# Kernel optimization log

Measured on AMD Instinct MI355X. Metric: run time of the kernel, lower is better.

Reference implementation:

```python
import jax, jax.numpy as jnp
import numpy as np

HID = 256; NH = 8; DH = 32; NL = 2
NV = 20000; NT = 50000; NE = 100000; NC = 8; FIN = 64


def setup_inputs() -> dict:
    ks = jax.random.split(jax.random.key(0), 32)
    f = lambda i, sh, s: jax.random.normal(ks[i], sh, dtype=jnp.float32) * s
    return {
        "x_v": f(0, (NV, FIN), 1.0),
        "x_t": f(1, (NT, FIN), 1.0),
        "ei_vt_src": jax.random.randint(ks[2], (NE,), 0, NV),
        "ei_vt_dst": jax.random.randint(ks[3], (NE,), 0, NT),
        "ei_tv_src": jax.random.randint(ks[4], (NE,), 0, NT),
        "ei_tv_dst": jax.random.randint(ks[5], (NE,), 0, NV),
        "ei_tt_src": jax.random.randint(ks[6], (NE,), 0, NT),
        "ei_tt_dst": jax.random.randint(ks[7], (NE,), 0, NT),
        "current": jax.random.randint(ks[8], (NC, 2), 0, NV),
        "W_in_v": f(9, (FIN, HID), 0.05), "b_in_v": jnp.zeros((HID,)),
        "W_in_t": f(10, (FIN, HID), 0.05), "b_in_t": jnp.zeros((HID,)),
        "Wk": f(11, (NL, 2, HID, HID), 0.05), "bk": jnp.zeros((NL, 2, HID)),
        "Wq": f(12, (NL, 2, HID, HID), 0.05), "bq": jnp.zeros((NL, 2, HID)),
        "Wv": f(13, (NL, 2, HID, HID), 0.05), "bv": jnp.zeros((NL, 2, HID)),
        "Wa": f(14, (NL, 2, HID, HID), 0.05), "ba": jnp.zeros((NL, 2, HID)),
        "skip": jnp.zeros((NL, 2)),
        "a_rel": f(15, (NL, 3, NH, DH, DH), 0.1),
        "m_rel": f(16, (NL, 3, NH, DH, DH), 0.1),
        "p_rel": jnp.ones((NL, 3, NH)),
        "Ws1": f(17, (2 * HID, HID), 0.05), "bs1": jnp.zeros((HID,)),
        "Ws2": f(18, (HID, 2), 0.05), "bs2": jnp.zeros((2,)),
    }


def reference(x_v, x_t, ei_vt_src, ei_vt_dst, ei_tv_src, ei_tv_dst,
              ei_tt_src, ei_tt_dst, current,
              W_in_v, b_in_v, W_in_t, b_in_t,
              Wk, bk, Wq, bq, Wv, bv, Wa, ba, skip,
              a_rel, m_rel, p_rel, Ws1, bs1, Ws2, bs2):
    scale = 1.0 / jnp.sqrt(jnp.float32(DH))
    # input projections + relu (lin_dict)
    hv = jax.nn.relu(x_v @ W_in_v + b_in_v)
    ht = jax.nn.relu(x_t @ W_in_t + b_in_t)
    # edge types: (src_type, dst_type, rel_idx, src_idx, dst_idx); 0=vehicle, 1=track
    edges = [(0, 1, 0, ei_vt_src, ei_vt_dst),
             (1, 0, 1, ei_tv_src, ei_tv_dst),
             (1, 1, 2, ei_tt_src, ei_tt_dst)]
    for l in range(NL):
        h = (hv, ht)
        proj = lambda W, b, t: (h[t] @ W[l, t] + b[l, t]).reshape(-1, NH, DH)
        k = (proj(Wk, bk, 0), proj(Wk, bk, 1))
        q = (proj(Wq, bq, 0), proj(Wq, bq, 1))
        v = (proj(Wv, bv, 0), proj(Wv, bv, 1))
        agg = [jnp.zeros((NV, NH, DH), jnp.float32),
               jnp.zeros((NT, NH, DH), jnp.float32)]
        for (st, dt, r, si, di) in edges:
            nd = agg[dt].shape[0]
            ke = jnp.einsum('ehd,hdf->ehf', k[st][si], a_rel[l, r])  # [E,H,D]
            ve = jnp.einsum('ehd,hdf->ehf', v[st][si], m_rel[l, r])  # [E,H,D]
            logit = (q[dt][di] * ke).sum(-1) * p_rel[l, r] * scale    # [E,H]
            m = jax.ops.segment_max(logit, di, num_segments=nd)
            e = jnp.exp(logit - m[di])
            s = jax.ops.segment_sum(e, di, num_segments=nd)
            alpha = e / (s[di] + 1e-16)
            agg[dt] = agg[dt] + jax.ops.segment_sum(alpha[..., None] * ve, di,
                                                    num_segments=nd)
        new = []
        for t in (0, 1):
            o = jax.nn.gelu(agg[t].reshape(-1, HID), approximate=False) @ Wa[l, t] + ba[l, t]
            beta = jax.nn.sigmoid(skip[l, t])
            new.append(beta * o + (1.0 - beta) * h[t])
        hv, ht = new
    # batched Scorer over (current vehicles) x (all tracks); cat([track, vehicle])
    veh = hv[current[:, 0]]                 # [C,HID]
    tpart = ht @ Ws1[:HID]                  # [NT,HID]
    vpart = veh @ Ws1[HID:] + bs1           # [C,HID]
    hmid = jax.nn.relu(tpart[None, :, :] + vpart[:, None, :])  # [C,NT,HID]
    out = hmid @ Ws2 + bs2                  # [C,NT,2]
    return out[..., 0], jax.nn.sigmoid(out[..., 1])
```

## Files before the change

### kernel.cpp

```cpp
#include <hip/hip_runtime.h>
#include <hip/hip_bf16.h>
#include <math.h>

#define HID 256
#define NH 8
#define DH 32
#define NL 2
#define NV 20000
#define NT 50000
#define NE 100000
#define NC 8
#define FIN 64

typedef unsigned short u16;
typedef unsigned int u32;
typedef short s16x8 __attribute__((ext_vector_type(8)));
typedef float f32x4 __attribute__((ext_vector_type(4)));

__device__ __forceinline__ float bf2f(u16 u) { return __uint_as_float(((u32)u) << 16); }
__device__ __forceinline__ u16 f2bf(float f) {
    u32 x = __float_as_uint(f);
    u32 r = ((x >> 16) & 1u) + 0x7fffu;
    return (u16)((x + r) >> 16);
}
__device__ __forceinline__ void up2(u32 u, float& a, float& b) {
    a = __uint_as_float(u << 16);
    b = __uint_as_float(u & 0xffff0000u);
}
__device__ __forceinline__ s16x8 gelu8(s16x8 a) {
    s16x8 r;
#pragma unroll
    for (int i = 0; i < 8; i++) {
        float v = bf2f((u16)a[i]);
        v = 0.5f * v * (1.f + erff(v * 0.70710678118654752f));
        r[i] = (short)f2bf(v);
    }
    return r;
}

__global__ void k_zero_i(int* __restrict__ p, int n) {
    for (int i = blockIdx.x * 256 + threadIdx.x; i < n; i += gridDim.x * 256) p[i] = 0;
}

__global__ void k_hist3(const int* __restrict__ d0, const int* __restrict__ d1, const int* __restrict__ d2,
                        int* __restrict__ cnt3) {
    int r = blockIdx.x >> 9;
    int b = blockIdx.x & 511;
    const int* dst = (r == 0) ? d0 : (r == 1) ? d1 : d2;
    int* cnt = cnt3 + (size_t)r * NT;
    for (int e = b * 256 + threadIdx.x; e < NE; e += 512 * 256)
        atomicAdd(&cnt[dst[e]], 1);
}

__global__ __launch_bounds__(1024) void k_scan3(const int* __restrict__ cnt3,
                                                int* __restrict__ rp0, int* __restrict__ rp1, int* __restrict__ rp2) {
    int r = blockIdx.x;
    const int* cnt = cnt3 + (size_t)r * NT;
    int* rp = (r == 0) ? rp0 : (r == 1) ? rp1 : rp2;
    int n = (r == 1) ? NV : NT;
    __shared__ int wsum[16];
    __shared__ int carry_s;
    int t = threadIdx.x, lane = t & 63, wv = t >> 6;
    if (t == 0) { carry_s = 0; rp[0] = 0; }
    __syncthreads();
    for (int base = 0; base < n; base += 1024) {
        int v = (base + t < n) ? cnt[base + t] : 0;
        int x = v;
#pragma unroll
        for (int off = 1; off < 64; off <<= 1) {
            int y = __shfl_up(x, off, 64);
            if (lane >= off) x += y;
        }
        if (lane == 63) wsum[wv] = x;
        __syncthreads();
        if (wv == 0 && lane < 16) {
            int s = wsum[lane];
#pragma unroll
            for (int off = 1; off < 16; off <<= 1) {
                int y = __shfl_up(s, off, 64);
                if (lane >= off) s += y;
            }
            wsum[lane] = s;
        }
        __syncthreads();
        int prefix = carry_s + (wv > 0 ? wsum[wv - 1] : 0);
        if (base + t < n) rp[base + t + 1] = prefix + x;
        __syncthreads();
        if (t == 0) carry_s += wsum[15];
        __syncthreads();
    }
}

__global__ void k_copy3(const int* __restrict__ rp0, const int* __restrict__ rp1, const int* __restrict__ rp2,
                        int* __restrict__ fill3) {
    int r = blockIdx.x >> 8;
    int b = blockIdx.x & 255;
    const int* rp = (r == 0) ? rp0 : (r == 1) ? rp1 : rp2;
    int n = (r == 1) ? NV : NT;
    int* fill = fill3 + (size_t)r * NT;
    for (int i = b * 256 + threadIdx.x; i < n; i += 256 * 256) fill[i] = rp[i];
}

__global__ void k_scatter3(const int* __restrict__ d0, const int* __restrict__ s0,
                           const int* __restrict__ d1, const int* __restrict__ s1,
                           const int* __restrict__ d2, const int* __restrict__ s2,
                           int* __restrict__ fill3,
                           int* __restrict__ es0, int* __restrict__ es1, int* __restrict__ es2) {
    int r = blockIdx.x >> 9;
    int b = blockIdx.x & 511;
    const int* dst = (r == 0) ? d0 : (r == 1) ? d1 : d2;
    const int* src = (r == 0) ? s0 : (r == 1) ? s1 : s2;
    int* fill = fill3 + (size_t)r * NT;
    int* es = (r == 0) ? es0 : (r == 1) ? es1 : es2;
    for (int e = b * 256 + threadIdx.x; e < NE; e += 512 * 256) {
        int d = dst[e];
        int p = atomicAdd(&fill[d], 1);
        es[p] = src[e];
    }
}

__global__ __launch_bounds__(256) void k_in_proj(const float* __restrict__ X, const float* __restrict__ W,
                          const float* __restrict__ b, u16* __restrict__ Y, int N) {
    const int NPB = 16;
    __shared__ float xs[NPB][FIN];
    int n0 = blockIdx.x * NPB;
    int t = threadIdx.x;
    for (int idx = t; idx < NPB * FIN; idx += 256) {
        int i = idx >> 6, c = idx & 63;
        int n = n0 + i;
        xs[i][c] = (n < N) ? X[(size_t)n * FIN + c] : 0.f;
    }
    __syncthreads();
    float acc[NPB];
#pragma unroll
    for (int i = 0; i < NPB; i++) acc[i] = 0.f;
    for (int c = 0; c < FIN; c++) {
        float w = W[c * HID + t];
#pragma unroll
        for (int i = 0; i < NPB; i++) acc[i] += xs[i][c] * w;
    }
    float bb = b[t];
    for (int i = 0; i < NPB; i++) {
        int n = n0 + i;
        if (n < N) Y[(size_t)n * HID + t] = f2bf(fmaxf(acc[i] + bb, 0.f));
    }
}

__device__ __forceinline__ int swz_idx(int k, int n) {
    int ks = k >> 5, r = k & 31;
    int j = r & 7;
    int l = ((r >> 3) << 4) | (n & 15);
    int nt = n >> 4;
    return ((ks * 16 + nt) * 64 + l) * 8 + j;
}

__global__ __launch_bounds__(256) void k_fuse_w2(
        const float* __restrict__ Wk_, const float* __restrict__ bk_, const float* __restrict__ Rk,
        u16* __restrict__ WswK, float* __restrict__ bkO,
        const float* __restrict__ Wv_, const float* __restrict__ bv_, const float* __restrict__ Rv,
        u16* __restrict__ WswV, float* __restrict__ bvO) {
    int h = blockIdx.x & 7;
    int which = blockIdx.x >> 3;
    const float* W = which ? Wv_ : Wk_;
    const float* b = which ? bv_ : bk_;
    const float* R = which ? Rv : Rk;
    u16* Wsw = which ? WswV : WswK;
    float* bout = which ? bvO : bkO;
    __shared__ float sR[DH * DH];
    int t = threadIdx.x;
    for (int idx = t; idx < DH * DH; idx += 256) sR[idx] = R[h * DH * DH + idx];
    __syncthreads();
    int f = t & 31, c0 = t >> 5;
    for (int c = c0; c < HID; c += 8) {
        float acc = 0.f;
#pragma unroll
        for (int d = 0; d < DH; d++) acc += W[c * HID + h * DH + d] * sR[d * DH + f];
        Wsw[swz_idx(c, h * DH + f)] = f2bf(acc);
    }
    if (t < DH) {
        float acc = 0.f;
#pragma unroll
        for (int d = 0; d < DH; d++) acc += b[h * DH + d] * sR[d * DH + t];
        bout[h * DH + t] = acc;
    }
}

__global__ __launch_bounds__(256) void k_swz_multi(const float* __restrict__ Wq, const float* __restrict__ Wa,
                                                   const float* __restrict__ Ws1, u16* __restrict__ out) {
    int slot = blockIdx.x >> 8;
    int idx = ((blockIdx.x & 255) << 8) | threadIdx.x;
    const float* src = (slot < 4) ? (Wq + (size_t)slot * 65536)
                     : (slot < 8) ? (Wa + (size_t)(slot - 4) * 65536)
                                  : Ws1;
    int j = idx & 7, l = (idx >> 3) & 63, nt = (idx >> 9) & 15, ks = idx >> 13;
    int k = ks * 32 + (l >> 4) * 8 + j;
    int n = nt * 16 + (l & 15);
    out[(size_t)slot * 65536 + idx] = f2bf(src[k * HID + n]);
}

template <int MODE, int GELU>
__global__ __launch_bounds__(256) void k_mm(const u16* __restrict__ X, const u16* __restrict__ Wsw,
                                            const float* __restrict__ bias, void* __restrict__ Y,
                                            const float* __restrict__ skip_, int N) {
    int tid = threadIdx.x;
    int w = tid >> 6, lane = tid & 63;
    int r0 = blockIdx.x * 16;
    int rA = r0 + (lane & 15);
    int koffg = lane >> 4;
    s16x8 a[8];
    if (rA < N) {
        const s16x8* ap = (const s16x8*)(X + (size_t)rA * HID) + koffg;
#pragma unroll
        for (int ks = 0; ks < 8; ks++) a[ks] = ap[ks * 4];
    } else {
#pragma unroll
        for (int ks = 0; ks < 8; ks++) a[ks] = (s16x8){0, 0, 0, 0, 0, 0, 0, 0};
    }
    if (GELU) {
#pragma unroll
        for (int ks = 0; ks < 8; ks++) a[ks] = gelu8(a[ks]);
    }
    f32x4 acc[4];
#pragma unroll
    for (int nt = 0; nt < 4; nt++) acc[nt] = (f32x4){0.f, 0.f, 0.f, 0.f};
    const s16x8* wp = (const s16x8*)Wsw;
#pragma unroll
    for (int ks = 0; ks < 8; ks++) {
        const s16x8* wq = wp + (size_t)ks * 16 * 64 + lane;
#pragma unroll
        for (int nt = 0; nt < 4; nt++) {
            s16x8 b = wq[(w * 4 + nt) * 64];
            acc[nt] = __builtin_amdgcn_mfma_f32_16x16x32_bf16(a[ks], b, acc[nt], 0, 0, 0);
        }
    }
    int colb = lane & 15;
    int rowb = r0 + koffg * 4;
    float beta = 0.f, ombeta = 0.f;
    if (MODE == 2) { beta = 1.f / (1.f + expf(-skip_[0])); ombeta = 1.f - beta; }
#pragma unroll
    for (int nt = 0; nt < 4; nt++) {
        int col = w * 64 + nt * 16 + colb;
        float bb = (MODE == 1 || MODE == 3) ? 0.f : bias[col];
#pragma unroll
        for (int j = 0; j < 4; j++) {
            int row = rowb + j;
            if (row < N) {
                float v = acc[nt][j] + bb;
                if (MODE == 0 || MODE == 3) {
                    ((u16*)Y)[(size_t)row * HID + col] = f2bf(v);
                } else if (MODE == 1) {
                    ((float*)Y)[(size_t)row * HID + col] = v;
                } else {
                    u16* hp = (u16*)Y + (size_t)row * HID + col;
                    *hp = f2bf(beta * v + ombeta * bf2f(*hp));
                }
            }
        }
    }
}

__global__ __launch_bounds__(256) void k_mm_gt(const u16* __restrict__ agg, const u16* __restrict__ WaSw,
                                               const float* __restrict__ ba_, const float* __restrict__ skip_,
                                               const u16* __restrict__ ht_old, const u16* __restrict__ Ws1Sw,
                                               u16* __restrict__ tpart, int N) {
    __shared__ u16 sH[16][264];
    int tid = threadIdx.x;
    int w = tid >> 6, lane = tid & 63;
    int r0 = blockIdx.x * 16;
    int rA = r0 + (lane & 15);
    int koffg = lane >> 4;
    s16x8 a[8];
    {
        const s16x8* ap = (const s16x8*)(agg + (size_t)rA * HID) + koffg;
#pragma unroll
        for (int ks = 0; ks < 8; ks++) a[ks] = gelu8(ap[ks * 4]);
    }
    f32x4 acc[4];
#pragma unroll
    for (int nt = 0; nt < 4; nt++) acc[nt] = (f32x4){0.f, 0.f, 0.f, 0.f};
    const s16x8* wp = (const s16x8*)WaSw;
#pragma unroll
    for (int ks = 0; ks < 8; ks++) {
        const s16x8* wq = wp + (size_t)ks * 16 * 64 + lane;
#pragma unroll
        for (int nt = 0; nt < 4; nt++)
            acc[nt] = __builtin_amdgcn_mfma_f32_16x16x32_bf16(a[ks], wq[(w * 4 + nt) * 64], acc[nt], 0, 0, 0);
    }
    float beta = 1.f / (1.f + expf(-skip_[0])), ombeta = 1.f - beta;
    int colb = lane & 15;
    int rowl = koffg * 4;
#pragma unroll
    for (int nt = 0; nt < 4; nt++) {
        int col = w * 64 + nt * 16 + colb;
        float bb = ba_[col];
#pragma unroll
        for (int j = 0; j < 4; j++) {
            int row = r0 + rowl + j;
            float v = acc[nt][j] + bb;
            float o = beta * v + ombeta * bf2f(ht_old[(size_t)row * HID + col]);
            sH[rowl + j][col] = f2bf(o);
        }
    }
    __syncthreads();
    s16x8 a2[8];
#pragma unroll
    for (int ks = 0; ks < 8; ks++)
        a2[ks] = *(const s16x8*)&sH[lane & 15][ks * 32 + koffg * 8];
#pragma unroll
    for (int nt = 0; nt < 4; nt++) acc[nt] = (f32x4){0.f, 0.f, 0.f, 0.f};
    const s16x8* wp2 = (const s16x8*)Ws1Sw;
#pragma unroll
    for (int ks = 0; ks < 8; ks++) {
        const s16x8* wq = wp2 + (size_t)ks * 16 * 64 + lane;
#pragma unroll
        for (int nt = 0; nt < 4; nt++)
            acc[nt] = __builtin_amdgcn_mfma_f32_16x16x32_bf16(a2[ks], wq[(w * 4 + nt) * 64], acc[nt], 0, 0, 0);
    }
#pragma unroll
    for (int nt = 0; nt < 4; nt++) {
        int col = w * 64 + nt * 16 + colb;
#pragma unroll
        for (int j = 0; j < 4; j++) {
            int row = r0 + rowl + j;
            if (row < N) tpart[(size_t)row * HID + col] = f2bf(acc[nt][j]);
        }
    }
}

__global__ __launch_bounds__(256) void k_mm_dv(const u16* __restrict__ aggv, const u16* __restrict__ WaSw,
                                               const float* __restrict__ ba_, const float* __restrict__ skip_,
                                               u16* __restrict__ hv,
                                               const u16* __restrict__ WkSw, const float* __restrict__ bkF,
                                               const u16* __restrict__ WvSw, const float* __restrict__ bvF,
                                               u16* __restrict__ kA0, u16* __restrict__ vM0, int N) {
    __shared__ u16 sH[16][264];
    int tid = threadIdx.x;
    int w = tid >> 6, lane = tid & 63;
    int r0 = blockIdx.x * 16;
    int rA = r0 + (lane & 15);
    int koffg = lane >> 4;
    s16x8 a[8];
    {
        const s16x8* ap = (const s16x8*)(aggv + (size_t)rA * HID) + koffg;
#pragma unroll
        for (int ks = 0; ks < 8; ks++) a[ks] = gelu8(ap[ks * 4]);
    }
    f32x4 acc[4];
#pragma unroll
    for (int nt = 0; nt < 4; nt++) acc[nt] = (f32x4){0.f, 0.f, 0.f, 0.f};
    const s16x8* wp = (const s16x8*)WaSw;
#pragma unroll
    for (int ks = 0; ks < 8; ks++) {
        const s16x8* wq = wp + (size_t)ks * 16 * 64 + lane;
#pragma unroll
        for (int nt = 0; nt < 4; nt++)
            acc[nt] = __builtin_amdgcn_mfma_f32_16x16x32_bf16(a[ks], wq[(w * 4 + nt) * 64], acc[nt], 0, 0, 0);
    }
    float beta = 1.f / (1.f + expf(-skip_[0])), ombeta = 1.f - beta;
    int colb = lane & 15;
    int rowl = koffg * 4;
#pragma unroll
    for (int nt = 0; nt < 4; nt++) {
        int col = w * 64 + nt * 16 + colb;
        float bb = ba_[col];
#pragma unroll
        for (int j = 0; j < 4; j++) {
            int row = r0 + rowl + j;
            float v = acc[nt][j] + bb;
            u16 o = f2bf(beta * v + ombeta * bf2f(hv[(size_t)row * HID + col]));
            hv[(size_t)row * HID + col] = o;
            sH[rowl + j][col] = o;
        }
    }
    __syncthreads();
    s16x8 a2[8];
#pragma unroll
    for (int ks = 0; ks < 8; ks++)
        a2[ks] = *(const s16x8*)&sH[lane & 15][ks * 32 + koffg * 8];
#pragma unroll
    for (int pass = 0; pass < 2; pass++) {
        const u16* Wsw = pass ? WvSw : WkSw;
        const float* bias = pass ? bvF : bkF;
        u16* Y = pass ? vM0 : kA0;
#pragma unroll
        for (int nt = 0; nt < 4; nt++) acc[nt] = (f32x4){0.f, 0.f, 0.f, 0.f};
        const s16x8* wp2 = (const s16x8*)Wsw;
#pragma unroll
        for (int ks = 0; ks < 8; ks++) {
            const s16x8* wq = wp2 + (size_t)ks * 16 * 64 + lane;
#pragma unroll
            for (int nt = 0; nt < 4; nt++)
                acc[nt] = __builtin_amdgcn_mfma_f32_16x16x32_bf16(a2[ks], wq[(w * 4 + nt) * 64], acc[nt], 0, 0, 0);
        }
#pragma unroll
        for (int nt = 0; nt < 4; nt++) {
            int col = w * 64 + nt * 16 + colb;
            float bb = bias[col];
#pragma unroll
            for (int j = 0; j < 4; j++) {
                int row = r0 + rowl + j;
                if (row < N) Y[(size_t)row * HID + col] = f2bf(acc[nt][j] + bb);
            }
        }
    }
}

__global__ __launch_bounds__(256) void k_mm2(const u16* __restrict__ X,
                                             const u16* __restrict__ W1, const float* __restrict__ b1, u16* __restrict__ Y1,
                                             const u16* __restrict__ W2, const float* __restrict__ b2, u16* __restrict__ Y2,
                                             int N) {
    int tid = threadIdx.x;
    int w = tid >> 6, lane = tid & 63;
    int r0 = blockIdx.x * 16;
    int rA = r0 + (lane & 15);
    int koffg = lane >> 4;
    s16x8 a[8];
    if (rA < N) {
        const s16x8* ap = (const s16x8*)(X + (size_t)rA * HID) + koffg;
#pragma unroll
        for (int ks = 0; ks < 8; ks++) a[ks] = ap[ks * 4];
    } else {
#pragma unroll
        for (int ks = 0; ks < 8; ks++) a[ks] = (s16x8){0, 0, 0, 0, 0, 0, 0, 0};
    }
    int colb = lane & 15;
    int rowb = r0 + koffg * 4;
#pragma unroll
    for (int pass = 0; pass < 2; pass++) {
        const u16* Wsw = pass ? W2 : W1;
        const float* bias = pass ? b2 : b1;
        u16* Y = pass ? Y2 : Y1;
        f32x4 acc[4];
#pragma unroll
        for (int nt = 0; nt < 4; nt++) acc[nt] = (f32x4){0.f, 0.f, 0.f, 0.f};
        const s16x8* wp = (const s16x8*)Wsw;
#pragma unroll
        for (int ks = 0; ks < 8; ks++) {
            const s16x8* wq = wp + (size_t)ks * 16 * 64 + lane;
#pragma unroll
            for (int nt = 0; nt < 4; nt++) {
                s16x8 b = wq[(w * 4 + nt) * 64];
                acc[nt] = __builtin_amdgcn_mfma_f32_16x16x32_bf16(a[ks], b, acc[nt], 0, 0, 0);
            }
        }
#pragma unroll
        for (int nt = 0; nt < 4; nt++) {
            int col = w * 64 + nt * 16 + colb;
            float bb = bias[col];
#pragma unroll
            for (int j = 0; j < 4; j++) {
                int row = rowb + j;
                if (row < N) Y[(size_t)row * HID + col] = f2bf(acc[nt][j] + bb);
            }
        }
    }
}

__global__ __launch_bounds__(256) void k_mm3(const u16* __restrict__ X,
                                             const u16* __restrict__ W0, const float* __restrict__ b0, u16* __restrict__ Y0,
                                             const u16* __restrict__ W1, const float* __restrict__ b1, u16* __restrict__ Y1,
                                             const u16* __restrict__ W2, const float* __restrict__ b2, u16* __restrict__ Y2,
                                             int N) {
    int tid = threadIdx.x;
    int w = tid >> 6, lane = tid & 63;
    int r0 = blockIdx.x * 16;
    int rA = r0 + (lane & 15);
    int koffg = lane >> 4;
    s16x8 a[8];
    if (rA < N) {
        const s16x8* ap = (const s16x8*)(X + (size_t)rA * HID) + koffg;
#pragma unroll
        for (int ks = 0; ks < 8; ks++) a[ks] = ap[ks * 4];
    } else {
#pragma unroll
        for (int ks = 0; ks < 8; ks++) a[ks] = (s16x8){0, 0, 0, 0, 0, 0, 0, 0};
    }
    int colb = lane & 15;
    int rowb = r0 + koffg * 4;
#pragma unroll
    for (int pass = 0; pass < 3; pass++) {
        const u16* Wsw = (pass == 0) ? W0 : (pass == 1) ? W1 : W2;
        const float* bias = (pass == 0) ? b0 : (pass == 1) ? b1 : b2;
        u16* Y = (pass == 0) ? Y0 : (pass == 1) ? Y1 : Y2;
        f32x4 acc[4];
#pragma unroll
        for (int nt = 0; nt < 4; nt++) acc[nt] = (f32x4){0.f, 0.f, 0.f, 0.f};
        const s16x8* wp = (const s16x8*)Wsw;
#pragma unroll
        for (int ks = 0; ks < 8; ks++) {
            const s16x8* wq = wp + (size_t)ks * 16 * 64 + lane;
#pragma unroll
            for (int nt = 0; nt < 4; nt++) {
                s16x8 b = wq[(w * 4 + nt) * 64];
                acc[nt] = __builtin_amdgcn_mfma_f32_16x16x32_bf16(a[ks], b, acc[nt], 0, 0, 0);
            }
        }
#pragma unroll
        for (int nt = 0; nt < 4; nt++) {
            int col = w * 64 + nt * 16 + colb;
            float bb = bias[col];
#pragma unroll
            for (int j = 0; j < 4; j++) {
                int row = rowb + j;
                if (row < N) Y[(size_t)row * HID + col] = f2bf(acc[nt][j] + bb);
            }
        }
    }
}

__device__ __forceinline__ void attn_pass(const u16* __restrict__ kA, const u16* __restrict__ vM,
                                          const int* __restrict__ es, int jb, int je,
                                          float q0, float q1, float q2, float q3, float ph, int lane4,
                                          float& o0, float& o1, float& o2, float& o3) {
    float m = -INFINITY, ss = 0.f, a0 = 0.f, a1 = 0.f, a2 = 0.f, a3 = 0.f;
    uint2 ku0 = {0, 0}, vu0 = {0, 0}, ku1 = {0, 0}, vu1 = {0, 0};
    if (jb < je) {
        int s = es[jb];
        ku0 = *(const uint2*)(kA + (size_t)s * HID + lane4);
        vu0 = *(const uint2*)(vM + (size_t)s * HID + lane4);
    }
    if (jb + 1 < je) {
        int s = es[jb + 1];
        ku1 = *(const uint2*)(kA + (size_t)s * HID + lane4);
        vu1 = *(const uint2*)(vM + (size_t)s * HID + lane4);
    }
    for (int j = jb; j < je; j++) {
        uint2 ku = ku0, vu = vu0;
        ku0 = ku1; vu0 = vu1;
        if (j + 2 < je) {
            int s = es[j + 2];
            ku1 = *(const uint2*)(kA + (size_t)s * HID + lane4);
            vu1 = *(const uint2*)(vM + (size_t)s * HID + lane4);
        }
        float k0, k1, k2, k3; up2(ku.x, k0, k1); up2(ku.y, k2, k3);
        float part = q0 * k0 + q1 * k1 + q2 * k2 + q3 * k3;
        part += __shfl_xor(part, 1, 64);
        part += __shfl_xor(part, 2, 64);
        part += __shfl_xor(part, 4, 64);
        float logit = part * ph;
        float nm = fmaxf(m, logit);
        float corr = expf(m - nm);
        float ee = expf(logit - nm);
        float v0, v1, v2, v3; up2(vu.x, v0, v1); up2(vu.y, v2, v3);
        ss = ss * corr + ee;
        a0 = a0 * corr + ee * v0; a1 = a1 * corr + ee * v1;
        a2 = a2 * corr + ee * v2; a3 = a3 * corr + ee * v3;
        m = nm;
    }
    float inv = 1.f / (ss + 1e-16f);
    o0 += a0 * inv; o1 += a1 * inv; o2 += a2 * inv; o3 += a3 * inv;
}

__global__ __launch_bounds__(256) void k_node_attn(
        const u16* __restrict__ q, const u16* __restrict__ kA, const u16* __restrict__ vM,
        const int* __restrict__ rp, const int* __restrict__ es,
        const float* __restrict__ P, float scale,
        u16* __restrict__ agg, int Nd) {
    int node = blockIdx.x * 4 + (threadIdx.x >> 6);
    if (node >= Nd) return;
    int lane = threadIdx.x & 63;
    float ph = P[lane >> 3] * scale;
    uint2 qu = *(const uint2*)(q + (size_t)node * HID + lane * 4);
    float q0, q1, q2, q3; up2(qu.x, q0, q1); up2(qu.y, q2, q3);
    float o0 = 0.f, o1 = 0.f, o2 = 0.f, o3 = 0.f;
    attn_pass(kA, vM, es, rp[node], rp[node + 1], q0, q1, q2, q3, ph, lane * 4, o0, o1, o2, o3);
    u16* ap = agg + (size_t)node * HID + lane * 4;
    ap[0] = f2bf(o0); ap[1] = f2bf(o1); ap[2] = f2bf(o2); ap[3] = f2bf(o3);
}

__global__ __launch_bounds__(256) void k_attn8(
        const u16* __restrict__ q8, const u16* __restrict__ kA, const u16* __restrict__ vM,
        const int* __restrict__ rp, const int* __restrict__ es, const int* __restrict__ current,
        const float* __restrict__ P, float scale, u16* __restrict__ agg8) {
    int wv = blockIdx.x * 4 + (threadIdx.x >> 6);
    if (wv >= NC) return;
    int node = current[wv * 2];
    int lane = threadIdx.x & 63;
    int lane4 = lane * 4;
    float ph = P[lane >> 3] * scale;
    uint2 qu = *(const uint2*)(q8 + (size_t)wv * HID + lane4);
    float q0, q1, q2, q3; up2(qu.x, q0, q1); up2(qu.y, q2, q3);
    float o0 = 0.f, o1 = 0.f, o2 = 0.f, o3 = 0.f;
    attn_pass(kA, vM, es, rp[node], rp[node + 1], q0, q1, q2, q3, ph, lane4, o0, o1, o2, o3);
    u16* ap = agg8 + (size_t)wv * HID + lane4;
    ap[0] = f2bf(o0); ap[1] = f2bf(o1); ap[2] = f2bf(o2); ap[3] = f2bf(o3);
}

__global__ __launch_bounds__(256) void k_q8(const u16* __restrict__ hv, const int* __restrict__ current,
                                            const float* __restrict__ Wq_, const float* __restrict__ bq_,
                                            u16* __restrict__ q8) {
    __shared__ float row[HID];
    int t = threadIdx.x;
    for (int c = 0; c < NC; c++) {
        int n = current[c * 2];
        row[t] = bf2f(hv[(size_t)n * HID + t]);
        __syncthreads();
        float acc = 0.f;
        for (int i = 0; i < HID; i++) acc += row[i] * Wq_[i * HID + t];
        q8[c * HID + t] = f2bf(acc + bq_[t]);
        __syncthreads();
    }
}

__global__ __launch_bounds__(256) void k_node_attn2(
        const u16* __restrict__ q,
        const u16* __restrict__ kA0, const u16* __restrict__ vM0,
        const int* __restrict__ rp0, const int* __restrict__ es0, const float* __restrict__ P0,
        const u16* __restrict__ kA1, const u16* __restrict__ vM1,
        const int* __restrict__ rp1, const int* __restrict__ es1, const float* __restrict__ P1,
        float scale, u16* __restrict__ agg, int Nd) {
    int node = blockIdx.x * 4 + (threadIdx.x >> 6);
    if (node >= Nd) return;
    int lane = threadIdx.x & 63;
    int h = lane >> 3;
    int lane4 = lane * 4;
    float ph0 = P0[h] * scale, ph1 = P1[h] * scale;
    uint2 qu = *(const uint2*)(q + (size_t)node * HID + lane4);
    float q0, q1, q2, q3; up2(qu.x, q0, q1); up2(qu.y, q2, q3);
    float o0 = 0.f, o1 = 0.f, o2 = 0.f, o3 = 0.f;
    attn_pass(kA0, vM0, es0, rp0[node], rp0[node + 1], q0, q1, q2, q3, ph0, lane4, o0, o1, o2, o3);
    attn_pass(kA1, vM1, es1, rp1[node], rp1[node + 1], q0, q1, q2, q3, ph1, lane4, o0, o1, o2, o3);
    u16* ap = agg + (size_t)node * HID + lane4;
    ap[0] = f2bf(o0); ap[1] = f2bf(o1); ap[2] = f2bf(o2); ap[3] = f2bf(o3);
}

__global__ __launch_bounds__(256) void k_vpart_f(
        const u16* __restrict__ agg8, const float* __restrict__ Wa_, const float* __restrict__ ba_,
        const float* __restrict__ skip_, const u16* __restrict__ hv, const int* __restrict__ current,
        const float* __restrict__ Ws1, const float* __restrict__ bs1, float* __restrict__ vpart) {
    __shared__ float sG[NC][HID];
    int t = threadIdx.x;
#pragma unroll
    for (int c = 0; c < NC; c++) {
        float x = bf2f(agg8[c * HID + t]);
        sG[c][t] = 0.5f * x * (1.f + erff(x * 0.70710678118654752f));
    }
    __syncthreads();
    float acc[NC];
#pragma unroll
    for (int c = 0; c < NC; c++) acc[c] = 0.f;
    for (int i = 0; i < HID; i++) {
        float wv_ = Wa_[i * HID + t];
#pragma unroll
        for (int c = 0; c < NC; c++) acc[c] += sG[c][i] * wv_;
    }
    float beta = 1.f / (1.f + expf(-skip_[0])), ombeta = 1.f - beta;
    float bb = ba_[t];
    __syncthreads();
#pragma unroll
    for (int c = 0; c < NC; c++) {
        int n = current[c * 2];
        float o = beta * (acc[c] + bb) + ombeta * bf2f(hv[(size_t)n * HID + t]);
        sG[c][t] = bf2f(f2bf(o));
    }
    __syncthreads();
    float acc2[NC];
#pragma unroll
    for (int c = 0; c < NC; c++) acc2[c] = 0.f;
    for (int i = 0; i < HID; i++) {
        float w1 = Ws1[(size_t)(HID + i) * HID + t];
#pragma unroll
        for (int c = 0; c < NC; c++) acc2[c] += sG[c][i] * w1;
    }
    float bs = bs1[t];
#pragma unroll
    for (int c = 0; c < NC; c++) vpart[c * HID + t] = acc2[c] + bs;
}

__global__ __launch_bounds__(256) void k_final(const u16* __restrict__ tpart, const float* __restrict__ vpart,
                        const float* __restrict__ Ws2, const float* __restrict__ bs2,
                        float* __restrict__ out) {
    __shared__ float vp[NC * HID];
    int t = threadIdx.x;
    for (int idx = t; idx < NC * HID; idx += 256) vp[idx] = vpart[idx];
    __syncthreads();
    int lane = t & 63, w = t >> 6;
    float w20[4], w21[4];
#pragma unroll
    for (int i = 0; i < 4; i++) {
        w20[i] = Ws2[(lane + 64 * i) * 2 + 0];
        w21[i] = Ws2[(lane + 64 * i) * 2 + 1];
    }
    float b0 = bs2[0], b1 = bs2[1];
    for (int n = blockIdx.x * 4 + w; n < NT; n += gridDim.x * 4) {
        float tp[4];
#pragma unroll
        for (int i = 0; i < 4; i++) tp[i] = bf2f(tpart[(size_t)n * HID + lane + 64 * i]);
#pragma unroll
        for (int c = 0; c < NC; c++) {
            float a0 = 0.f, a1 = 0.f;
#pragma unroll
            for (int i = 0; i < 4; i++) {
                float hm = fmaxf(tp[i] + vp[c * HID + lane + 64 * i], 0.f);
                a0 += hm * w20[i];
                a1 += hm * w21[i];
            }
#pragma unroll
            for (int off = 32; off >= 1; off >>= 1) {
                a0 += __shfl_xor(a0, off, 64);
                a1 += __shfl_xor(a1, off, 64);
            }
            if (lane == 0) {
                out[(size_t)c * NT + n] = a0 + b0;
                float z = a1 + b1;
                out[(size_t)NC * NT + (size_t)c * NT + n] = 1.f / (1.f + expf(-z));
            }
        }
    }
}

extern "C" void kernel_launch(void* const* d_in, const int* in_sizes, int n_in,
                              void* d_out, int out_size, void* d_ws, size_t ws_size,
                              hipStream_t stream) {
    (void)in_sizes; (void)n_in; (void)out_size;
    const float* x_v    = (const float*)d_in[0];
    const float* x_t    = (const float*)d_in[1];
    const int* ei_vt_s  = (const int*)d_in[2];
    const int* ei_vt_d  = (const int*)d_in[3];
    const int* ei_tv_s  = (const int*)d_in[4];
    const int* ei_tv_d  = (const int*)d_in[5];
    const int* ei_tt_s  = (const int*)d_in[6];
    const int* ei_tt_d  = (const int*)d_in[7];
    const int* current  = (const int*)d_in[8];
    const float* W_in_v = (const float*)d_in[9];
    const float* b_in_v = (const float*)d_in[10];
    const float* W_in_t = (const float*)d_in[11];
    const float* b_in_t = (const float*)d_in[12];
    const float* Wk     = (const float*)d_in[13];
    const float* bk     = (const float*)d_in[14];
    const float* Wq     = (const float*)d_in[15];
    const float* bq     = (const float*)d_in[16];
    const float* Wv     = (const float*)d_in[17];
    const float* bv     = (const float*)d_in[18];
    const float* Wa     = (const float*)d_in[19];
    const float* ba     = (const float*)d_in[20];
    const float* skip   = (const float*)d_in[21];
    const float* a_rel  = (const float*)d_in[22];
    const float* m_rel  = (const float*)d_in[23];
    const float* p_rel  = (const float*)d_in[24];
    const float* Ws1    = (const float*)d_in[25];
    const float* bs1    = (const float*)d_in[26];
    const float* Ws2    = (const float*)d_in[27];
    const float* bs2    = (const float*)d_in[28];

    char* p = (char*)d_ws;
    auto alloc = [&](size_t bytes) -> char* {
        char* r = p;
        p += (bytes + 255) & ~(size_t)255;
        return r;
    };
    u16* hv   = (u16*)alloc((size_t)NV * HID * 2);
    u16* ht   = (u16*)alloc((size_t)NT * HID * 2);
    u16* qb   = (u16*)alloc((size_t)NT * HID * 2);
    u16* qv   = (u16*)alloc((size_t)NV * HID * 2);
    u16* kA   = (u16*)alloc((size_t)NT * HID * 2);
    u16* vM   = (u16*)alloc((size_t)NT * HID * 2);
    u16* kA0  = (u16*)alloc((size_t)NV * HID * 2);
    u16* vM0  = (u16*)alloc((size_t)NV * HID * 2);
    u16* agg  = (u16*)alloc((size_t)NT * HID * 2);
    int* rp_vt = (int*)alloc((size_t)(NT + 1) * 4);
    int* rp_tv = (int*)alloc((size_t)(NV + 1) * 4);
    int* rp_tt = (int*)alloc((size_t)(NT + 1) * 4);
    int* es_vt = (int*)alloc((size_t)NE * 4);
    int* es_tv = (int*)alloc((size_t)NE * 4);
    int* es_tt = (int*)alloc((size_t)NE * 4);
    int* cnt3  = (int*)alloc((size_t)3 * NT * 4);
    int* fill3 = (int*)alloc((size_t)3 * NT * 4);
    float* vp  = (float*)alloc((size_t)NC * HID * 4);
    u16* q8   = (u16*)alloc((size_t)NC * HID * 2);
    u16* agg8 = (u16*)alloc((size_t)NC * HID * 2);
    float* bkF = (float*)alloc(HID * 4);
    float* bvF = (float*)alloc(HID * 4);
    u16*  wswK = (u16*)alloc((size_t)HID * HID * 2);
    u16*  wswV = (u16*)alloc((size_t)HID * HID * 2);
    u16*  wswK2 = (u16*)alloc((size_t)HID * HID * 2);
    u16*  wswV2 = (u16*)alloc((size_t)HID * HID * 2);
    float* bkF2 = (float*)alloc(HID * 4);
    float* bvF2 = (float*)alloc(HID * 4);
    u16*  wswA = (u16*)alloc((size_t)9 * HID * HID * 2);
    if ((size_t)(p - (char*)d_ws) > ws_size) return;

    const float scale = 0.17677669529663687f;

    k_zero_i<<<256, 256, 0, stream>>>(cnt3, 3 * NT);
    k_hist3<<<3 * 512, 256, 0, stream>>>(ei_vt_d, ei_tv_d, ei_tt_d, cnt3);
    k_scan3<<<3, 1024, 0, stream>>>(cnt3, rp_vt, rp_tv, rp_tt);
    k_copy3<<<3 * 256, 256, 0, stream>>>(rp_vt, rp_tv, rp_tt, fill3);
    k_scatter3<<<3 * 512, 256, 0, stream>>>(ei_vt_d, ei_vt_s, ei_tv_d, ei_tv_s, ei_tt_d, ei_tt_s,
                                            fill3, es_vt, es_tv, es_tt);
    k_swz_multi<<<9 * 256, 256, 0, stream>>>(Wq, Wa, Ws1, wswA);
    k_in_proj<<<(NV + 15) / 16, 256, 0, stream>>>(x_v, W_in_v, b_in_v, hv, NV);
    k_in_proj<<<(NT + 15) / 16, 256, 0, stream>>>(x_t, W_in_t, b_in_t, ht, NT);

    const int GV = (NV + 15) / 16, GT = (NT + 15) / 16;
    const float* AR = a_rel; const float* MR = m_rel;
#define REL_W(l, r) (AR + (size_t)((l) * 3 + (r)) * NH * DH * DH)
#define REL_M(l, r) (MR + (size_t)((l) * 3 + (r)) * NH * DH * DH)
#define REL_P(l, r) (p_rel + (size_t)((l) * 3 + (r)) * NH)

    k_fuse_w2<<<2 * NH, 256, 0, stream>>>(Wk + 0 * 65536, bk + 0 * HID, REL_W(0, 0), wswK, bkF,
                                          Wv + 0 * 65536, bv + 0 * HID, REL_M(0, 0), wswV, bvF);
    k_mm3<<<GV, 256, 0, stream>>>(hv, wswA + 0 * 65536, bq + 0 * HID, qv, wswK, bkF, kA0, wswV, bvF, vM0, NV);
    k_fuse_w2<<<2 * NH, 256, 0, stream>>>(Wk + 1 * 65536, bk + 1 * HID, REL_W(0, 1), wswK, bkF,
                                          Wv + 1 * 65536, bv + 1 * HID, REL_M(0, 1), wswV, bvF);
    k_mm3<<<GT, 256, 0, stream>>>(ht, wswA + 1 * 65536, bq + 1 * HID, qb, wswK, bkF, kA, wswV, bvF, vM, NT);
    k_node_attn<<<(NV + 3) / 4, 256, 0, stream>>>(qv, kA, vM, rp_tv, es_tv, REL_P(0, 1), scale, qv, NV);
    k_fuse_w2<<<2 * NH, 256, 0, stream>>>(Wk + 1 * 65536, bk + 1 * HID, REL_W(0, 2), wswK2, bkF2,
                                          Wv + 1 * 65536, bv + 1 * HID, REL_M(0, 2), wswV2, bvF2);
    k_mm2<<<GT, 256, 0, stream>>>(ht, wswK2, bkF2, kA, wswV2, bvF2, vM, NT);
    k_node_attn2<<<(NT + 3) / 4, 256, 0, stream>>>(qb, kA0, vM0, rp_vt, es_vt, REL_P(0, 0),
                                                   kA, vM, rp_tt, es_tt, REL_P(0, 2), scale, agg, NT);
    k_mm<2, 1><<<GT, 256, 0, stream>>>(agg, wswA + (size_t)(4 + 1) * 65536, ba + 1 * HID, ht, skip + 1, NT);

    k_fuse_w2<<<2 * NH, 256, 0, stream>>>(Wk + 2 * 65536, bk + 2 * HID, REL_W(1, 0), wswK, bkF,
                                          Wv + 2 * 65536, bv + 2 * HID, REL_M(1, 0), wswV, bvF);
    k_mm_dv<<<GV, 256, 0, stream>>>(qv , wswA + (size_t)(4 + 0) * 65536, ba + 0 * HID, skip + 0,
                                    hv, wswK, bkF, wswV, bvF, kA0, vM0, NV);
    k_q8<<<1, 256, 0, stream>>>(hv, current, Wq + (size_t)2 * 65536, bq + 2 * HID, q8);

    k_fuse_w2<<<2 * NH, 256, 0, stream>>>(Wk + 3 * 65536, bk + 3 * HID, REL_W(1, 1), wswK, bkF,
                                          Wv + 3 * 65536, bv + 3 * HID, REL_M(1, 1), wswV, bvF);
    k_mm3<<<GT, 256, 0, stream>>>(ht, wswA + 3 * 65536, bq + 3 * HID, qb, wswK, bkF, kA, wswV, bvF, vM, NT);
    k_attn8<<<2, 256, 0, stream>>>(q8, kA, vM, rp_tv, es_tv, current, REL_P(1, 1), scale, agg8);
    k_fuse_w2<<<2 * NH, 256, 0, stream>>>(Wk + 3 * 65536, bk + 3 * HID, REL_W(1, 2), wswK2, bkF2,
                                          Wv + 3 * 65536, bv + 3 * HID, REL_M(1, 2), wswV2, bvF2);
    k_mm2<<<GT, 256, 0, stream>>>(ht, wswK2, bkF2, kA, wswV2, bvF2, vM, NT);
    k_node_attn2<<<(NT + 3) / 4, 256, 0, stream>>>(qb, kA0, vM0, rp_vt, es_vt, REL_P(1, 0),
                                                   kA, vM, rp_tt, es_tt, REL_P(1, 2), scale, agg, NT);
    k_mm_gt<<<GT, 256, 0, stream>>>(agg, wswA + (size_t)(4 + 3) * 65536, ba + 3 * HID, skip + 3,
                                    ht, wswA + (size_t)8 * 65536, kA, NT);

    k_vpart_f<<<1, 256, 0, stream>>>(agg8, Wa + (size_t)2 * 65536, ba + 2 * HID, skip + 2,
                                     hv, current, Ws1, bs1, vp);
    k_final<<<2048, 256, 0, stream>>>(kA , vp, Ws2, bs2, (float*)d_out);
}
```

Measured before the change: 971.9 us.

## Fuse track output projection with next-layer Q/K/V projections in one kernel

Replaces the layer-0 track output GEMM plus the later layer-1 k_mm3 and k_mm2 launches with a single kernel. It computes the gated skip update of ht, keeps the new rows in shared memory, and immediately runs five projections (q, k and v for two relations). This avoids re-reading ht from global memory and cuts launches. It needs extra kB/vB buffers and reorders the weight-fusion launches. The larger kernel may raise register pressure.

```diff
diff --git a/kernel.cpp b/kernel.cpp
--- a/kernel.cpp
+++ b/kernel.cpp
@@ -198,67 +198,6 @@
     out[(size_t)slot * 65536 + idx] = f2bf(src[k * HID + n]);
 }
 
-template <int MODE, int GELU>
-__global__ __launch_bounds__(256) void k_mm(const u16* __restrict__ X, const u16* __restrict__ Wsw,
-                                            const float* __restrict__ bias, void* __restrict__ Y,
-                                            const float* __restrict__ skip_, int N) {
-    int tid = threadIdx.x;
-    int w = tid >> 6, lane = tid & 63;
-    int r0 = blockIdx.x * 16;
-    int rA = r0 + (lane & 15);
-    int koffg = lane >> 4;
-    s16x8 a[8];
-    if (rA < N) {
-        const s16x8* ap = (const s16x8*)(X + (size_t)rA * HID) + koffg;
-#pragma unroll
-        for (int ks = 0; ks < 8; ks++) a[ks] = ap[ks * 4];
-    } else {
-#pragma unroll
-        for (int ks = 0; ks < 8; ks++) a[ks] = (s16x8){0, 0, 0, 0, 0, 0, 0, 0};
-    }
-    if (GELU) {
-#pragma unroll
-        for (int ks = 0; ks < 8; ks++) a[ks] = gelu8(a[ks]);
-    }
-    f32x4 acc[4];
-#pragma unroll
-    for (int nt = 0; nt < 4; nt++) acc[nt] = (f32x4){0.f, 0.f, 0.f, 0.f};
-    const s16x8* wp = (const s16x8*)Wsw;
-#pragma unroll
-    for (int ks = 0; ks < 8; ks++) {
-        const s16x8* wq = wp + (size_t)ks * 16 * 64 + lane;
-#pragma unroll
-        for (int nt = 0; nt < 4; nt++) {
-            s16x8 b = wq[(w * 4 + nt) * 64];
-            acc[nt] = __builtin_amdgcn_mfma_f32_16x16x32_bf16(a[ks], b, acc[nt], 0, 0, 0);
-        }
-    }
-    int colb = lane & 15;
-    int rowb = r0 + koffg * 4;
-    float beta = 0.f, ombeta = 0.f;
-    if (MODE == 2) { beta = 1.f / (1.f + expf(-skip_[0])); ombeta = 1.f - beta; }
-#pragma unroll
-    for (int nt = 0; nt < 4; nt++) {
-        int col = w * 64 + nt * 16 + colb;
-        float bb = (MODE == 1 || MODE == 3) ? 0.f : bias[col];
-#pragma unroll
-        for (int j = 0; j < 4; j++) {
-            int row = rowb + j;
-            if (row < N) {
-                float v = acc[nt][j] + bb;
-                if (MODE == 0 || MODE == 3) {
-                    ((u16*)Y)[(size_t)row * HID + col] = f2bf(v);
-                } else if (MODE == 1) {
-                    ((float*)Y)[(size_t)row * HID + col] = v;
-                } else {
-                    u16* hp = (u16*)Y + (size_t)row * HID + col;
-                    *hp = f2bf(beta * v + ombeta * bf2f(*hp));
-                }
-            }
-        }
-    }
-}
-
 __global__ __launch_bounds__(256) void k_mm_gt(const u16* __restrict__ agg, const u16* __restrict__ WaSw,
                                                const float* __restrict__ ba_, const float* __restrict__ skip_,
                                                const u16* __restrict__ ht_old, const u16* __restrict__ Ws1Sw,
@@ -323,6 +262,91 @@
         for (int j = 0; j < 4; j++) {
             int row = r0 + rowl + j;
             if (row < N) tpart[(size_t)row * HID + col] = f2bf(acc[nt][j]);
+        }
+    }
+}
+
+__global__ __launch_bounds__(256) void k_mm_gt6(
+        const u16* __restrict__ agg, const u16* __restrict__ WaSw,
+        const float* __restrict__ ba_, const float* __restrict__ skip_,
+        u16* __restrict__ ht,
+        const u16* __restrict__ WqSw, const float* __restrict__ bq_,
+        const u16* __restrict__ Wk1Sw, const float* __restrict__ bk1_,
+        const u16* __restrict__ Wv1Sw, const float* __restrict__ bv1_,
+        const u16* __restrict__ Wk2Sw, const float* __restrict__ bk2_,
+        const u16* __restrict__ Wv2Sw, const float* __restrict__ bv2_,
+        u16* __restrict__ qb, u16* __restrict__ kA, u16* __restrict__ vM,
+        u16* __restrict__ kB, u16* __restrict__ vB, int N) {
+    __shared__ u16 sH[16][264];
+    int tid = threadIdx.x;
+    int w = tid >> 6, lane = tid & 63;
+    int r0 = blockIdx.x * 16;
+    int rA = r0 + (lane & 15);
+    int koffg = lane >> 4;
+    s16x8 a[8];
+    {
+        const s16x8* ap = (const s16x8*)(agg + (size_t)rA * HID) + koffg;
+#pragma unroll
+        for (int ks = 0; ks < 8; ks++) a[ks] = gelu8(ap[ks * 4]);
+    }
+    f32x4 acc[4];
+#pragma unroll
+    for (int nt = 0; nt < 4; nt++) acc[nt] = (f32x4){0.f, 0.f, 0.f, 0.f};
+    const s16x8* wp = (const s16x8*)WaSw;
+#pragma unroll
+    for (int ks = 0; ks < 8; ks++) {
+        const s16x8* wq = wp + (size_t)ks * 16 * 64 + lane;
+#pragma unroll
+        for (int nt = 0; nt < 4; nt++)
+            acc[nt] = __builtin_amdgcn_mfma_f32_16x16x32_bf16(a[ks], wq[(w * 4 + nt) * 64], acc[nt], 0, 0, 0);
+    }
+    float beta = 1.f / (1.f + expf(-skip_[0])), ombeta = 1.f - beta;
+    int colb = lane & 15;
+    int rowl = koffg * 4;
+#pragma unroll
+    for (int nt = 0; nt < 4; nt++) {
+        int col = w * 64 + nt * 16 + colb;
+        float bb = ba_[col];
+#pragma unroll
+        for (int j = 0; j < 4; j++) {
+            int row = r0 + rowl + j;
+            float v = acc[nt][j] + bb;
+            u16 o = f2bf(beta * v + ombeta * bf2f(ht[(size_t)row * HID + col]));
+            ht[(size_t)row * HID + col] = o;
+            sH[rowl + j][col] = o;
+        }
+    }
+    __syncthreads();
+    s16x8 a2[8];
+#pragma unroll
+    for (int ks = 0; ks < 8; ks++)
+        a2[ks] = *(const s16x8*)&sH[lane & 15][ks * 32 + koffg * 8];
+    const u16* Ws[5] = { WqSw, Wk1Sw, Wv1Sw, Wk2Sw, Wv2Sw };
+    const float* Bs[5] = { bq_, bk1_, bv1_, bk2_, bv2_ };
+    u16* Ys[5] = { qb, kA, vM, kB, vB };
+#pragma unroll
+    for (int pass = 0; pass < 5; pass++) {
+#pragma unroll
+        for (int nt = 0; nt < 4; nt++) acc[nt] = (f32x4){0.f, 0.f, 0.f, 0.f};
+        const s16x8* wp2 = (const s16x8*)Ws[pass];
+#pragma unroll
+        for (int ks = 0; ks < 8; ks++) {
+            const s16x8* wq = wp2 + (size_t)ks * 16 * 64 + lane;
+#pragma unroll
+            for (int nt = 0; nt < 4; nt++)
+                acc[nt] = __builtin_amdgcn_mfma_f32_16x16x32_bf16(a2[ks], wq[(w * 4 + nt) * 64], acc[nt], 0, 0, 0);
+        }
+        const float* bias = Bs[pass];
+        u16* Y = Ys[pass];
+#pragma unroll
+        for (int nt = 0; nt < 4; nt++) {
+            int col = w * 64 + nt * 16 + colb;
+            float bb = bias[col];
+#pragma unroll
+            for (int j = 0; j < 4; j++) {
+                int row = r0 + rowl + j;
+                if (row < N) Y[(size_t)row * HID + col] = f2bf(acc[nt][j] + bb);
+            }
         }
     }
 }
@@ -755,6 +779,8 @@
     u16* qv   = (u16*)alloc((size_t)NV * HID * 2);
     u16* kA   = (u16*)alloc((size_t)NT * HID * 2);
     u16* vM   = (u16*)alloc((size_t)NT * HID * 2);
+    u16* kB   = (u16*)alloc((size_t)NT * HID * 2);
+    u16* vB   = (u16*)alloc((size_t)NT * HID * 2);
     u16* kA0  = (u16*)alloc((size_t)NV * HID * 2);
     u16* vM0  = (u16*)alloc((size_t)NV * HID * 2);
     u16* agg  = (u16*)alloc((size_t)NT * HID * 2);
@@ -793,9 +819,8 @@
     k_in_proj<<<(NT + 15) / 16, 256, 0, stream>>>(x_t, W_in_t, b_in_t, ht, NT);
 
     const int GV = (NV + 15) / 16, GT = (NT + 15) / 16;
-    const float* AR = a_rel; const float* MR = m_rel;
-#define REL_W(l, r) (AR + (size_t)((l) * 3 + (r)) * NH * DH * DH)
-#define REL_M(l, r) (MR + (size_t)((l) * 3 + (r)) * NH * DH * DH)
+#define REL_W(l, r) (a_rel + (size_t)((l) * 3 + (r)) * NH * DH * DH)
+#define REL_M(l, r) (m_rel + (size_t)((l) * 3 + (r)) * NH * DH * DH)
 #define REL_P(l, r) (p_rel + (size_t)((l) * 3 + (r)) * NH)
 
     k_fuse_w2<<<2 * NH, 256, 0, stream>>>(Wk + 0 * 65536, bk + 0 * HID, REL_W(0, 0), wswK, bkF,
@@ -810,7 +835,17 @@
     k_mm2<<<GT, 256, 0, stream>>>(ht, wswK2, bkF2, kA, wswV2, bvF2, vM, NT);
     k_node_attn2<<<(NT + 3) / 4, 256, 0, stream>>>(qb, kA0, vM0, rp_vt, es_vt, REL_P(0, 0),
                                                    kA, vM, rp_tt, es_tt, REL_P(0, 2), scale, agg, NT);
-    k_mm<2, 1><<<GT, 256, 0, stream>>>(agg, wswA + (size_t)(4 + 1) * 65536, ba + 1 * HID, ht, skip + 1, NT);
+
+    k_fuse_w2<<<2 * NH, 256, 0, stream>>>(Wk + 3 * 65536, bk + 3 * HID, REL_W(1, 1), wswK, bkF,
+                                          Wv + 3 * 65536, bv + 3 * HID, REL_M(1, 1), wswV, bvF);
+    k_fuse_w2<<<2 * NH, 256, 0, stream>>>(Wk + 3 * 65536, bk + 3 * HID, REL_W(1, 2), wswK2, bkF2,
+                                          Wv + 3 * 65536, bv + 3 * HID, REL_M(1, 2), wswV2, bvF2);
+    k_mm_gt6<<<GT, 256, 0, stream>>>(agg, wswA + (size_t)(4 + 1) * 65536, ba + 1 * HID, skip + 1,
+                                     ht,
+                                     wswA + 3 * 65536, bq + 3 * HID,
+                                     wswK, bkF, wswV, bvF,
+                                     wswK2, bkF2, wswV2, bvF2,
+                                     qb, kA, vM, kB, vB, NT);
 
     k_fuse_w2<<<2 * NH, 256, 0, stream>>>(Wk + 2 * 65536, bk + 2 * HID, REL_W(1, 0), wswK, bkF,
                                           Wv + 2 * 65536, bv + 2 * HID, REL_M(1, 0), wswV, bvF);
@@ -818,15 +853,9 @@
                                     hv, wswK, bkF, wswV, bvF, kA0, vM0, NV);
     k_q8<<<1, 256, 0, stream>>>(hv, current, Wq + (size_t)2 * 65536, bq + 2 * HID, q8);
 
-    k_fuse_w2<<<2 * NH, 256, 0, stream>>>(Wk + 3 * 65536, bk + 3 * HID, REL_W(1, 1), wswK, bkF,
-                                          Wv + 3 * 65536, bv + 3 * HID, REL_M(1, 1), wswV, bvF);
-    k_mm3<<<GT, 256, 0, stream>>>(ht, wswA + 3 * 65536, bq + 3 * HID, qb, wswK, bkF, kA, wswV, bvF, vM, NT);
     k_attn8<<<2, 256, 0, stream>>>(q8, kA, vM, rp_tv, es_tv, current, REL_P(1, 1), scale, agg8);
-    k_fuse_w2<<<2 * NH, 256, 0, stream>>>(Wk + 3 * 65536, bk + 3 * HID, REL_W(1, 2), wswK2, bkF2,
-                                          Wv + 3 * 65536, bv + 3 * HID, REL_M(1, 2), wswV2, bvF2);
-    k_mm2<<<GT, 256, 0, stream>>>(ht, wswK2, bkF2, kA, wswV2, bvF2, vM, NT);
     k_node_attn2<<<(NT + 3) / 4, 256, 0, stream>>>(qb, kA0, vM0, rp_vt, es_vt, REL_P(1, 0),
-                                                   kA, vM, rp_tt, es_tt, REL_P(1, 2), scale, agg, NT);
+                                                   kB, vB, rp_tt, es_tt, REL_P(1, 2), scale, agg, NT);
     k_mm_gt<<<GT, 256, 0, stream>>>(agg, wswA + (size_t)(4 + 3) * 65536, ba + 3 * HID, skip + 3,
                                     ht, wswA + (size_t)8 * 65536, kA, NT);
 
```

Measured after the change: 997.6 us. +2.6%, slower.
